# Kernel optimization log

Measured on AMD Instinct MI355X. Metric: run time of the kernel, lower is better.

The kernel has to match this reference:

```python
import jax, jax.numpy as jnp
import numpy as np

N_VERTICES = 50000
N_FEATURES = 128
N_EDGES = 640000


def setup_inputs() -> dict:
    key = jax.random.key(0)
    k1, k2, k3, k4 = jax.random.split(key, 4)
    inp = jax.random.normal(k1, (N_VERTICES, N_FEATURES), dtype=jnp.float32)
    eidx = jax.random.randint(k2, (2, N_EDGES), 0, N_VERTICES, dtype=jnp.int64)
    enorm = jax.random.uniform(k3, (N_EDGES,), dtype=jnp.float32)
    esgn = jnp.sign(jax.random.normal(k4, (N_EDGES,), dtype=jnp.float32))
    return {"input": inp, "eidx": eidx, "enorm": enorm, "esgn": esgn}


def reference(input, eidx, enorm, esgn):
    sidx, tidx = eidx[0], eidx[1]
    # gather source node features, scale by signed normalized edge weight
    message = input[sidx] * (esgn * enorm)[:, None]  # [n_edges, d]
    # scatter-add messages onto target nodes
    res = jax.ops.segment_sum(message, tidx, num_segments=input.shape[0])
    return res
```

## Files before the change

kernel.cpp:

```cpp
#include <hip/hip_runtime.h>


#define N_V 50000
#define N_F 128
#define N_E 640000
#define CAP 64

__global__ void __launch_bounds__(256) gc_atomic_fallback(
    const float* __restrict__ input, const int* __restrict__ sidx,
    const int* __restrict__ tidx, const float* __restrict__ enorm,
    const float* __restrict__ esgn, float* __restrict__ out)
{
    const int e = blockIdx.x * 8 + (threadIdx.x >> 5);
    if (e >= N_E) return;
    const int lane = threadIdx.x & 31;
    const int s = sidx[e], t = tidx[e];
    const float w = esgn[e] * enorm[e];
    float4 v = reinterpret_cast<const float4*>(input + (size_t)s * N_F)[lane];
    float* orow = out + (size_t)t * N_F + lane * 4;
    atomicAdd(orow + 0, v.x * w);
    atomicAdd(orow + 1, v.y * w);
    atomicAdd(orow + 2, v.z * w);
    atomicAdd(orow + 3, v.w * w);
}

__global__ void __launch_bounds__(256) gc_scatter_packed(
    const int* __restrict__ sidx, const int* __restrict__ tidx,
    const float* __restrict__ enorm, const float* __restrict__ esgn,
    int* __restrict__ cnt, int2* __restrict__ bucket)
{
    const int e = blockIdx.x * 256 + threadIdx.x;
    if (e >= N_E) return;
    const int t = tidx[e];
    const int pos = atomicAdd(&cnt[t], 1);
    if (pos < CAP) {
        const float w = esgn[e] * enorm[e];
        bucket[t * CAP + pos] = make_int2(sidx[e], __float_as_int(w));
    }
}

__global__ void __launch_bounds__(256) gc_gather_packed(
    const float* __restrict__ input, const int* __restrict__ cnt,
    const int2* __restrict__ bucket, float* __restrict__ out)
{
    const int v = blockIdx.x * 4 + (threadIdx.x >> 6);
    if (v >= N_V) return;
    const int lane = threadIdx.x & 63;

    const int n = min(cnt[v], CAP);
    int2 rec = (lane < n) ? bucket[v * CAP + lane] : make_int2(0, 0);
    const float w_l = __int_as_float(rec.y);

    float2 acc0 = make_float2(0.f, 0.f);
    float2 acc1 = make_float2(0.f, 0.f);
    int k = 0;
    for (; k + 1 < n; k += 2) {
        const int   s0 = __shfl(rec.x, k);
        const float w0 = __shfl(w_l, k);
        const int   s1 = __shfl(rec.x, k + 1);
        const float w1 = __shfl(w_l, k + 1);
        const float2 x0 = *reinterpret_cast<const float2*>(
            input + (size_t)s0 * N_F + lane * 2);
        const float2 x1 = *reinterpret_cast<const float2*>(
            input + (size_t)s1 * N_F + lane * 2);
        acc0.x += x0.x * w0; acc0.y += x0.y * w0;
        acc1.x += x1.x * w1; acc1.y += x1.y * w1;
    }
    if (k < n) {
        const int   s0 = __shfl(rec.x, k);
        const float w0 = __shfl(w_l, k);
        const float2 x0 = *reinterpret_cast<const float2*>(
            input + (size_t)s0 * N_F + lane * 2);
        acc0.x += x0.x * w0; acc0.y += x0.y * w0;
    }
    acc0.x += acc1.x; acc0.y += acc1.y;
    *reinterpret_cast<float2*>(out + (size_t)v * N_F + lane * 2) = acc0;
}

__global__ void __launch_bounds__(256) gc_scatter_eid(
    const int* __restrict__ tidx, int* __restrict__ cnt, int* __restrict__ bucket)
{
    const int e = blockIdx.x * 256 + threadIdx.x;
    if (e >= N_E) return;
    const int t = tidx[e];
    const int pos = atomicAdd(&cnt[t], 1);
    if (pos < CAP) bucket[t * CAP + pos] = e;
}

__global__ void __launch_bounds__(256) gc_gather_eid(
    const float* __restrict__ input, const int* __restrict__ sidx,
    const float* __restrict__ enorm, const float* __restrict__ esgn,
    const int* __restrict__ cnt, const int* __restrict__ bucket,
    float* __restrict__ out)
{
    const int v = blockIdx.x * 4 + (threadIdx.x >> 6);
    if (v >= N_V) return;
    const int lane = threadIdx.x & 63;

    const int n = min(cnt[v], CAP);
    const int e_l = (lane < n) ? bucket[v * CAP + lane] : 0;
    const int s_l = (lane < n) ? sidx[e_l] : 0;
    const float w_l = (lane < n) ? (esgn[e_l] * enorm[e_l]) : 0.f;

    float2 acc = make_float2(0.f, 0.f);
    for (int k = 0; k < n; ++k) {
        const int   s = __shfl(s_l, k);
        const float w = __shfl(w_l, k);
        const float2 x = *reinterpret_cast<const float2*>(
            input + (size_t)s * N_F + lane * 2);
        acc.x += x.x * w;
        acc.y += x.y * w;
    }
    *reinterpret_cast<float2*>(out + (size_t)v * N_F + lane * 2) = acc;
}

extern "C" void kernel_launch(void* const* d_in, const int* in_sizes, int n_in,
                              void* d_out, int out_size, void* d_ws, size_t ws_size,
                              hipStream_t stream) {
    const float* input = (const float*)d_in[0];
    const int*   eidx  = (const int*)d_in[1];
    const float* enorm = (const float*)d_in[2];
    const float* esgn  = (const float*)d_in[3];
    float* out = (float*)d_out;

    const int* sidx = eidx;
    const int* tidx = eidx + N_E;

    const int eb = (N_E + 255) / 256;
    const int vb = (N_V + 3) / 4;

    const size_t needA = (size_t)N_V * sizeof(int) + (size_t)N_V * CAP * sizeof(int2);
    const size_t needB = (size_t)N_V * sizeof(int) + (size_t)N_V * CAP * sizeof(int);

    if (ws_size >= needA) {
        int*  cnt    = (int*)d_ws;
        int2* bucket = (int2*)(cnt + N_V);
        hipMemsetAsync(cnt, 0, (size_t)N_V * sizeof(int), stream);
        hipLaunchKernelGGL(gc_scatter_packed, dim3(eb), dim3(256), 0, stream,
                           sidx, tidx, enorm, esgn, cnt, bucket);
        hipLaunchKernelGGL(gc_gather_packed, dim3(vb), dim3(256), 0, stream,
                           input, cnt, bucket, out);
    } else if (ws_size >= needB) {
        int* cnt    = (int*)d_ws;
        int* bucket = cnt + N_V;
        hipMemsetAsync(cnt, 0, (size_t)N_V * sizeof(int), stream);
        hipLaunchKernelGGL(gc_scatter_eid, dim3(eb), dim3(256), 0, stream,
                           tidx, cnt, bucket);
        hipLaunchKernelGGL(gc_gather_eid, dim3(vb), dim3(256), 0, stream,
                           input, sidx, enorm, esgn, cnt, bucket, out);
    } else {
        hipMemsetAsync(d_out, 0, (size_t)out_size * sizeof(float), stream);
        hipLaunchKernelGGL(gc_atomic_fallback, dim3(N_E / 8), dim3(256), 0,
                           stream, input, sidx, tidx, enorm, esgn, out);
    }
}
```

Baseline: 157.9 us.

## Fuse memset, scatter and gather into one cooperative persistent kernel

Replaces the memset plus two-kernel bucket pipeline with a single cooperative kernel of 1024 blocks that zeroes counts, scatters packed edge records into per-vertex buckets, and gathers, separated by grid-wide syncs. The goal is to remove launch overhead and the inter-kernel gaps. In exchange it adds two grid barriers, and the gather phase loops over vertices with a fixed persistent grid. The eid-based middle path is removed, and the old path remains as a fallback if the cooperative launch fails.

```diff
diff --git a/kernel.cpp b/kernel.cpp
--- a/kernel.cpp
+++ b/kernel.cpp
@@ -1,27 +1,73 @@
 #include <hip/hip_runtime.h>
+#include <hip/hip_cooperative_groups.h>
+
+namespace cg = cooperative_groups;
 
 
 #define N_V 50000
 #define N_F 128
 #define N_E 640000
 #define CAP 64
+#define NBLK 1024
+#define NTHR 256
 
-__global__ void __launch_bounds__(256) gc_atomic_fallback(
-    const float* __restrict__ input, const int* __restrict__ sidx,
-    const int* __restrict__ tidx, const float* __restrict__ enorm,
-    const float* __restrict__ esgn, float* __restrict__ out)
+__global__ void __launch_bounds__(NTHR, 4) gc_fused(
+    const float* __restrict__ input,
+    const int* __restrict__ sidx, const int* __restrict__ tidx,
+    const float* __restrict__ enorm, const float* __restrict__ esgn,
+    int* __restrict__ cnt, int2* __restrict__ bucket,
+    float* __restrict__ out)
 {
-    const int e = blockIdx.x * 8 + (threadIdx.x >> 5);
-    if (e >= N_E) return;
-    const int lane = threadIdx.x & 31;
-    const int s = sidx[e], t = tidx[e];
-    const float w = esgn[e] * enorm[e];
-    float4 v = reinterpret_cast<const float4*>(input + (size_t)s * N_F)[lane];
-    float* orow = out + (size_t)t * N_F + lane * 4;
-    atomicAdd(orow + 0, v.x * w);
-    atomicAdd(orow + 1, v.y * w);
-    atomicAdd(orow + 2, v.z * w);
-    atomicAdd(orow + 3, v.w * w);
+    cg::grid_group grid = cg::this_grid();
+    const int tid = blockIdx.x * NTHR + threadIdx.x;
+    const int nthreads = NBLK * NTHR;
+
+    for (int i = tid; i < N_V; i += nthreads) cnt[i] = 0;
+    grid.sync();
+
+    for (int e = tid; e < N_E; e += nthreads) {
+        const int t = tidx[e];
+        const int pos = atomicAdd(&cnt[t], 1);
+        if (pos < CAP) {
+            const float w = esgn[e] * enorm[e];
+            bucket[(size_t)t * CAP + pos] = make_int2(sidx[e], __float_as_int(w));
+        }
+    }
+    grid.sync();
+
+    const int wave = tid >> 6;
+    const int lane = tid & 63;
+    const int nwaves = nthreads >> 6;
+    for (int v = wave; v < N_V; v += nwaves) {
+        const int n = min(cnt[v], CAP);
+        int2 rec = (lane < n) ? bucket[(size_t)v * CAP + lane] : make_int2(0, 0);
+        const float w_l = __int_as_float(rec.y);
+
+        float2 acc0 = make_float2(0.f, 0.f);
+        float2 acc1 = make_float2(0.f, 0.f);
+        int k = 0;
+        for (; k + 1 < n; k += 2) {
+            const int   s0 = __shfl(rec.x, k);
+            const float w0 = __shfl(w_l, k);
+            const int   s1 = __shfl(rec.x, k + 1);
+            const float w1 = __shfl(w_l, k + 1);
+            const float2 x0 = *reinterpret_cast<const float2*>(
+                input + (size_t)s0 * N_F + lane * 2);
+            const float2 x1 = *reinterpret_cast<const float2*>(
+                input + (size_t)s1 * N_F + lane * 2);
+            acc0.x += x0.x * w0; acc0.y += x0.y * w0;
+            acc1.x += x1.x * w1; acc1.y += x1.y * w1;
+        }
+        if (k < n) {
+            const int   s0 = __shfl(rec.x, k);
+            const float w0 = __shfl(w_l, k);
+            const float2 x0 = *reinterpret_cast<const float2*>(
+                input + (size_t)s0 * N_F + lane * 2);
+            acc0.x += x0.x * w0; acc0.y += x0.y * w0;
+        }
+        acc0.x += acc1.x; acc0.y += acc1.y;
+        *reinterpret_cast<float2*>(out + (size_t)v * N_F + lane * 2) = acc0;
+    }
 }
 
 __global__ void __launch_bounds__(256) gc_scatter_packed(
@@ -35,7 +81,7 @@
     const int pos = atomicAdd(&cnt[t], 1);
     if (pos < CAP) {
         const float w = esgn[e] * enorm[e];
-        bucket[t * CAP + pos] = make_int2(sidx[e], __float_as_int(w));
+        bucket[(size_t)t * CAP + pos] = make_int2(sidx[e], __float_as_int(w));
     }
 }
 
@@ -46,11 +92,9 @@
     const int v = blockIdx.x * 4 + (threadIdx.x >> 6);
     if (v >= N_V) return;
     const int lane = threadIdx.x & 63;
-
     const int n = min(cnt[v], CAP);
-    int2 rec = (lane < n) ? bucket[v * CAP + lane] : make_int2(0, 0);
+    int2 rec = (lane < n) ? bucket[(size_t)v * CAP + lane] : make_int2(0, 0);
     const float w_l = __int_as_float(rec.y);
-
     float2 acc0 = make_float2(0.f, 0.f);
     float2 acc1 = make_float2(0.f, 0.f);
     int k = 0;
@@ -77,41 +121,22 @@
     *reinterpret_cast<float2*>(out + (size_t)v * N_F + lane * 2) = acc0;
 }
 
-__global__ void __launch_bounds__(256) gc_scatter_eid(
-    const int* __restrict__ tidx, int* __restrict__ cnt, int* __restrict__ bucket)
+__global__ void __launch_bounds__(256) gc_atomic_fallback(
+    const float* __restrict__ input, const int* __restrict__ sidx,
+    const int* __restrict__ tidx, const float* __restrict__ enorm,
+    const float* __restrict__ esgn, float* __restrict__ out)
 {
-    const int e = blockIdx.x * 256 + threadIdx.x;
+    const int e = blockIdx.x * 8 + (threadIdx.x >> 5);
     if (e >= N_E) return;
-    const int t = tidx[e];
-    const int pos = atomicAdd(&cnt[t], 1);
-    if (pos < CAP) bucket[t * CAP + pos] = e;
-}
-
-__global__ void __launch_bounds__(256) gc_gather_eid(
-    const float* __restrict__ input, const int* __restrict__ sidx,
-    const float* __restrict__ enorm, const float* __restrict__ esgn,
-    const int* __restrict__ cnt, const int* __restrict__ bucket,
-    float* __restrict__ out)
-{
-    const int v = blockIdx.x * 4 + (threadIdx.x >> 6);
-    if (v >= N_V) return;
-    const int lane = threadIdx.x & 63;
-
-    const int n = min(cnt[v], CAP);
-    const int e_l = (lane < n) ? bucket[v * CAP + lane] : 0;
-    const int s_l = (lane < n) ? sidx[e_l] : 0;
-    const float w_l = (lane < n) ? (esgn[e_l] * enorm[e_l]) : 0.f;
-
-    float2 acc = make_float2(0.f, 0.f);
-    for (int k = 0; k < n; ++k) {
-        const int   s = __shfl(s_l, k);
-        const float w = __shfl(w_l, k);
-        const float2 x = *reinterpret_cast<const float2*>(
-            input + (size_t)s * N_F + lane * 2);
-        acc.x += x.x * w;
-        acc.y += x.y * w;
-    }
-    *reinterpret_cast<float2*>(out + (size_t)v * N_F + lane * 2) = acc;
+    const int lane = threadIdx.x & 31;
+    const int s = sidx[e], t = tidx[e];
+    const float w = esgn[e] * enorm[e];
+    float4 v = reinterpret_cast<const float4*>(input + (size_t)s * N_F)[lane];
+    float* orow = out + (size_t)t * N_F + lane * 4;
+    atomicAdd(orow + 0, v.x * w);
+    atomicAdd(orow + 1, v.y * w);
+    atomicAdd(orow + 2, v.z * w);
+    atomicAdd(orow + 3, v.w * w);
 }
 
 extern "C" void kernel_launch(void* const* d_in, const int* in_sizes, int n_in,
@@ -126,28 +151,24 @@
     const int* sidx = eidx;
     const int* tidx = eidx + N_E;
 
-    const int eb = (N_E + 255) / 256;
-    const int vb = (N_V + 3) / 4;
+    const size_t need = (size_t)N_V * sizeof(int) + (size_t)N_V * CAP * sizeof(int2);
 
-    const size_t needA = (size_t)N_V * sizeof(int) + (size_t)N_V * CAP * sizeof(int2);
-    const size_t needB = (size_t)N_V * sizeof(int) + (size_t)N_V * CAP * sizeof(int);
-
-    if (ws_size >= needA) {
+    if (ws_size >= need) {
         int*  cnt    = (int*)d_ws;
         int2* bucket = (int2*)(cnt + N_V);
+
+        void* args[] = {(void*)&input, (void*)&sidx, (void*)&tidx,
+                        (void*)&enorm, (void*)&esgn,
+                        (void*)&cnt, (void*)&bucket, (void*)&out};
+        hipError_t err = hipLaunchCooperativeKernel(
+            (const void*)gc_fused, dim3(NBLK), dim3(NTHR), args, 0, stream);
+        if (err == hipSuccess) return;
+
         hipMemsetAsync(cnt, 0, (size_t)N_V * sizeof(int), stream);
-        hipLaunchKernelGGL(gc_scatter_packed, dim3(eb), dim3(256), 0, stream,
-                           sidx, tidx, enorm, esgn, cnt, bucket);
-        hipLaunchKernelGGL(gc_gather_packed, dim3(vb), dim3(256), 0, stream,
-                           input, cnt, bucket, out);
-    } else if (ws_size >= needB) {
-        int* cnt    = (int*)d_ws;
-        int* bucket = cnt + N_V;
-        hipMemsetAsync(cnt, 0, (size_t)N_V * sizeof(int), stream);
-        hipLaunchKernelGGL(gc_scatter_eid, dim3(eb), dim3(256), 0, stream,
-                           tidx, cnt, bucket);
-        hipLaunchKernelGGL(gc_gather_eid, dim3(vb), dim3(256), 0, stream,
-                           input, sidx, enorm, esgn, cnt, bucket, out);
+        hipLaunchKernelGGL(gc_scatter_packed, dim3((N_E + 255) / 256), dim3(256),
+                           0, stream, sidx, tidx, enorm, esgn, cnt, bucket);
+        hipLaunchKernelGGL(gc_gather_packed, dim3((N_V + 3) / 4), dim3(256),
+                           0, stream, input, cnt, bucket, out);
     } else {
         hipMemsetAsync(d_out, 0, (size_t)out_size * sizeof(float), stream);
         hipLaunchKernelGGL(gc_atomic_fallback, dim3(N_E / 8), dim3(256), 0,
```

After: 350.7 us. 2.22x slower.
